# Kernel tuning notes

Hardware: AMD Instinct MI355X
Metric: run time of the kernel (lower is better)

## Reference

```python
import jax, jax.numpy as jnp
import numpy as np

N, F, H, R, E = 50000, 128, 128, 8, 800000
BN_EPS = 1e-5


def setup_inputs() -> dict:
    key = jax.random.key(0)
    ks = jax.random.split(key, 10)
    g = lambda k, shp: jax.random.normal(k, shp, dtype=jnp.float32) * (1.0 / np.sqrt(shp[-2] if len(shp) > 1 else shp[-1]))
    return {
        "x": jax.random.normal(ks[0], (N, F), dtype=jnp.float32),
        "edge_index": jax.random.randint(ks[1], (2, E), 0, N, dtype=jnp.int32),
        "edge_type": jax.random.randint(ks[2], (E,), 0, R, dtype=jnp.int32),
        "W1": g(ks[3], (F, H)),
        "b1": jnp.zeros((H,), jnp.float32),
        "weight": g(ks[4], (R, H, H)),
        "root": g(ks[5], (H, H)),
        "bias_c": jnp.zeros((H,), jnp.float32),
        "gamma": jnp.ones((H,), jnp.float32),
        "beta": jnp.zeros((H,), jnp.float32),
        "W2": g(ks[6], (H, H)),
        "b2": jnp.zeros((H,), jnp.float32),
        "Wo": g(ks[7], (H, 1)),
        "bo": jnp.zeros((1,), jnp.float32),
    }


def reference(x, edge_index, edge_type, W1, b1, weight, root, bias_c, gamma, beta, W2, b2, Wo, bo):
    n = x.shape[0]
    r = weight.shape[0]
    src, dst = edge_index[0], edge_index[1]
    # segment id combining relation and destination node: equivalent to the
    # per-relation edge-mask + scatter-add loop in RGCNConv, but in one pass.
    seg = edge_type.astype(jnp.int32) * n + dst

    def conv(h):
        msg = h[src]                                            # [E, H] gather
        agg = jax.ops.segment_sum(msg, seg, num_segments=r * n)  # [R*N, H]
        agg = agg.reshape(r, n, -1)                             # [R, N, H]
        out = jnp.einsum('rnc,rco->no', agg, weight)            # per-relation matmul, summed
        return out + h @ root + bias_c

    def bn(h):
        mu = h.mean(axis=0)
        var = h.var(axis=0)  # biased var, matches torch BN training normalization
        return gamma * (h - mu) * jax.lax.rsqrt(var + BN_EPS) + beta

    h = x @ W1 + b1
    h = jax.nn.relu(bn(conv(h)))
    h = jax.nn.relu(bn(conv(h)))
    h = h @ W2 + b2
    h = h @ Wo + bo
    return jax.nn.sigmoid(h)
```

## Files before the change

kernel.cpp:

```cpp
#include <hip/hip_runtime.h>
#include <stdint.h>

typedef __bf16 bf16;
typedef __bf16 bf16x8 __attribute__((ext_vector_type(8)));
typedef float f32x4 __attribute__((ext_vector_type(4)));

__device__ __forceinline__ float bfbits2f(uint32_t lo16) {
    uint32_t b = lo16 << 16;
    float f;
    __builtin_memcpy(&f, &b, 4);
    return f;
}

__device__ __forceinline__ uint32_t pack2bf(float a, float b) {
    uint32_t lo = __builtin_bit_cast(unsigned short, (bf16)a);
    uint32_t hi = __builtin_bit_cast(unsigned short, (bf16)b);
    return lo | (hi << 16);
}

__device__ __forceinline__ void gload_lds16(const void* g, void* l) {
    __builtin_amdgcn_global_load_lds((const __attribute__((address_space(1))) void*)g,
                                     (__attribute__((address_space(3))) void*)l, 16, 0, 0);
}

__global__ void k_prep(const float* __restrict__ W1, const float* __restrict__ weight,
                       const float* __restrict__ root, const float* __restrict__ W2,
                       const float* __restrict__ b2, const float* __restrict__ Wo,
                       const float* __restrict__ bo, bf16* __restrict__ W1T,
                       bf16* __restrict__ WcatT2, float* __restrict__ qc, int R, int ldt) {
    int total = 16384 * (R + 2);
    for (int i = blockIdx.x * blockDim.x + threadIdx.x; i < total + 129; i += gridDim.x * blockDim.x) {
        if (i < 16384) {
            int f = i >> 7, h = i & 127;
            W1T[h * 128 + f] = (bf16)W1[f * 128 + h];
        } else if (i < total) {
            int j = i - 16384;
            int r = j >> 14, rem = j & 16383, c = rem >> 7, o = rem & 127;
            float v = (r < R) ? weight[(size_t)(r * 128 + c) * 128 + o] : root[c * 128 + o];
            WcatT2[(size_t)o * ldt + r * 128 + c] = (bf16)v;
        } else {
            int t = i - total;
            if (t < 128) {
                float s = 0.f;
                for (int j = 0; j < 128; j++) s += W2[t * 128 + j] * Wo[j];
                qc[t] = s;
            } else {
                float c = bo[0];
                for (int j = 0; j < 128; j++) c += b2[j] * Wo[j];
                qc[128] = c;
            }
        }
    }
}

__global__ void k_hist(const int* __restrict__ dst, int* __restrict__ cnt, int E) {
    for (int e = blockIdx.x * blockDim.x + threadIdx.x; e < E; e += gridDim.x * blockDim.x)
        atomicAdd(&cnt[dst[e]], 1);
}

__global__ __launch_bounds__(256) void k_scan_blk(const int* __restrict__ cnt, int* __restrict__ bsum, int N) {
    int i = blockIdx.x * 256 + threadIdx.x;
    int v = (i < N) ? cnt[i] : 0;
#pragma unroll
    for (int d = 1; d < 64; d <<= 1) v += __shfl_xor(v, d);
    __shared__ int ws[4];
    if ((threadIdx.x & 63) == 0) ws[threadIdx.x >> 6] = v;
    __syncthreads();
    if (threadIdx.x == 0) bsum[blockIdx.x] = ws[0] + ws[1] + ws[2] + ws[3];
}

__global__ __launch_bounds__(256) void k_scan_top(int* __restrict__ bsum, int nb) {
    __shared__ int s[256];
    int t = threadIdx.x;
    int v = (t < nb) ? bsum[t] : 0;
    s[t] = v;
    __syncthreads();
#pragma unroll
    for (int d = 1; d < 256; d <<= 1) {
        int u = (t >= d) ? s[t - d] : 0;
        __syncthreads();
        s[t] += u;
        __syncthreads();
    }
    if (t < nb) bsum[t] = s[t] - v;
}

__global__ __launch_bounds__(256) void k_scan_apply(const int* __restrict__ cnt, const int* __restrict__ bsum,
                                                    int* __restrict__ row_off, int* __restrict__ cursor, int N) {
    int b = blockIdx.x, t = threadIdx.x;
    int i = b * 256 + t;
    int v = (i < N) ? cnt[i] : 0;
    int lane = t & 63, wid = t >> 6;
    int incl = v;
#pragma unroll
    for (int d = 1; d < 64; d <<= 1) {
        int u = __shfl_up(incl, d);
        if (lane >= d) incl += u;
    }
    __shared__ int ws[4];
    if (lane == 63) ws[wid] = incl;
    __syncthreads();
    int woff = 0;
    for (int wj = 0; wj < 4; wj++)
        if (wj < wid) woff += ws[wj];
    int excl = bsum[b] + woff + incl - v;
    if (i < N) {
        row_off[i] = excl;
        cursor[i] = excl;
        if (i == N - 1) row_off[N] = excl + v;
    }
}

__global__ void k_fill(const int* __restrict__ src, const int* __restrict__ dst,
                       const int* __restrict__ etype, int* __restrict__ cursor,
                       int* __restrict__ csr, int E, int pbase) {
    int p = blockIdx.x & 7;
    int bg = blockIdx.x >> 3;
    int nchunk = gridDim.x >> 3;
    int chunk = (E + nchunk - 1) / nchunk;
    int beg = bg * chunk, end = min(beg + chunk, E);
    int lo = p * pbase, hi = lo + pbase;
    for (int e = beg + (int)threadIdx.x; e < end; e += blockDim.x) {
        int d = dst[e];
        if (d >= lo && d < hi) {
            int pos = atomicAdd(&cursor[d], 1);
            csr[pos] = (etype[e] << 16) | src[e];
        }
    }
}

__global__ __launch_bounds__(256) void k_gemm0(const float* __restrict__ A, const bf16* __restrict__ BT,
                                               const float* __restrict__ bias, bf16* __restrict__ C, int M) {
    __shared__ bf16 sA[128 * 128];
    __shared__ bf16 sB[128 * 128];
    int tid = threadIdx.x;
    int m0 = blockIdx.x * 128;
#pragma unroll
    for (int i = 0; i < 8; i++) {
        int chunk = i * 256 + tid;
        int row = chunk >> 4, c16 = chunk & 15;
        int sw = ((c16 ^ (row & 7)) << 3);
        int gr = m0 + row;
        int4 va = {0, 0, 0, 0};
        if (gr < M) {
            const float* ap = A + (size_t)gr * 128 + (c16 << 3);
            float4 f0 = *reinterpret_cast<const float4*>(ap);
            float4 f1 = *reinterpret_cast<const float4*>(ap + 4);
            bf16 tmp[8] = {(bf16)f0.x, (bf16)f0.y, (bf16)f0.z, (bf16)f0.w,
                           (bf16)f1.x, (bf16)f1.y, (bf16)f1.z, (bf16)f1.w};
            __builtin_memcpy(&va, tmp, 16);
        }
        *reinterpret_cast<int4*>(&sA[row * 128 + sw]) = va;
        int4 vb = *reinterpret_cast<const int4*>(&BT[(size_t)row * 128 + (c16 << 3)]);
        *reinterpret_cast<int4*>(&sB[row * 128 + sw]) = vb;
    }
    __syncthreads();

    int lane = tid & 63, w = tid >> 6;
    int wm = (w >> 1) * 64, wn = (w & 1) * 64;
    int lr = lane & 15, lk = lane >> 4;
    f32x4 zero = {0.f, 0.f, 0.f, 0.f};
    f32x4 acc[4][4];
#pragma unroll
    for (int mi = 0; mi < 4; mi++)
#pragma unroll
        for (int ni = 0; ni < 4; ni++) acc[mi][ni] = zero;

#pragma unroll
    for (int kk = 0; kk < 4; kk++) {
        int c = (kk << 2) + lk;
        bf16x8 af[4], bfr[4];
#pragma unroll
        for (int mi = 0; mi < 4; mi++) {
            int r = wm + mi * 16 + lr;
            af[mi] = *reinterpret_cast<const bf16x8*>(&sA[r * 128 + ((c ^ (r & 7)) << 3)]);
        }
#pragma unroll
        for (int ni = 0; ni < 4; ni++) {
            int r = wn + ni * 16 + lr;
            bfr[ni] = *reinterpret_cast<const bf16x8*>(&sB[r * 128 + ((c ^ (r & 7)) << 3)]);
        }
#pragma unroll
        for (int mi = 0; mi < 4; mi++)
#pragma unroll
            for (int ni = 0; ni < 4; ni++)
                acc[mi][ni] = __builtin_amdgcn_mfma_f32_16x16x32_bf16(af[mi], bfr[ni], acc[mi][ni], 0, 0, 0);
    }

#pragma unroll
    for (int ni = 0; ni < 4; ni++) {
        int col = wn + ni * 16 + lr;
        float bia = bias[col];
#pragma unroll
        for (int mi = 0; mi < 4; mi++) {
#pragma unroll
            for (int j = 0; j < 4; j++) {
                int row = m0 + wm + mi * 16 + lk * 4 + j;
                if (row < M) C[(size_t)row * 128 + col] = (bf16)(acc[mi][ni][j] + bia);
            }
        }
    }
}

__global__ __launch_bounds__(128) void k_agg2(const bf16* __restrict__ h, const int* __restrict__ row_off,
                                              const int* __restrict__ csr, bf16* __restrict__ G, int N) {
    __shared__ float acc[2][8 * 128];
    int wi = threadIdx.x >> 6;
    int n = blockIdx.x * 2 + wi;
    if (n >= N) return;
    int lane = threadIdx.x & 63;
    int c0 = lane * 2;
    float* a = acc[wi];
#pragma unroll
    for (int i = 0; i < 16; i++) a[i * 64 + lane] = 0.f;
    int beg = row_off[n], end = row_off[n + 1];
    int i = beg;
    for (; i + 4 <= end; i += 4) {
        int p0 = csr[i], p1 = csr[i + 1], p2 = csr[i + 2], p3 = csr[i + 3];
        uint32_t v0 = *reinterpret_cast<const uint32_t*>(&h[(size_t)(p0 & 0xffff) * 128 + c0]);
        uint32_t v1 = *reinterpret_cast<const uint32_t*>(&h[(size_t)(p1 & 0xffff) * 128 + c0]);
        uint32_t v2 = *reinterpret_cast<const uint32_t*>(&h[(size_t)(p2 & 0xffff) * 128 + c0]);
        uint32_t v3 = *reinterpret_cast<const uint32_t*>(&h[(size_t)(p3 & 0xffff) * 128 + c0]);
        float* a0 = &a[(p0 >> 16) * 128 + c0];
        a0[0] += bfbits2f(v0 & 0xffffu); a0[1] += bfbits2f(v0 >> 16);
        float* a1 = &a[(p1 >> 16) * 128 + c0];
        a1[0] += bfbits2f(v1 & 0xffffu); a1[1] += bfbits2f(v1 >> 16);
        float* a2 = &a[(p2 >> 16) * 128 + c0];
        a2[0] += bfbits2f(v2 & 0xffffu); a2[1] += bfbits2f(v2 >> 16);
        float* a3 = &a[(p3 >> 16) * 128 + c0];
        a3[0] += bfbits2f(v3 & 0xffffu); a3[1] += bfbits2f(v3 >> 16);
    }
    for (; i < end; i++) {
        int p = csr[i];
        uint32_t v = *reinterpret_cast<const uint32_t*>(&h[(size_t)(p & 0xffff) * 128 + c0]);
        float* ap = &a[(p >> 16) * 128 + c0];
        ap[0] += bfbits2f(v & 0xffffu);
        ap[1] += bfbits2f(v >> 16);
    }
    size_t gbase = (size_t)n * 1024 + c0;
#pragma unroll
    for (int r = 0; r < 8; r++) {
        __builtin_nontemporal_store(pack2bf(a[r * 128 + c0], a[r * 128 + c0 + 1]),
                                    reinterpret_cast<uint32_t*>(&G[gbase + r * 128]));
    }
}

__global__ __launch_bounds__(256) void k_gemm2(const bf16* __restrict__ G, const bf16* __restrict__ hsrc,
                                               const bf16* __restrict__ BT, const float* __restrict__ bias,
                                               float* __restrict__ C, float* __restrict__ stats,
                                               int M, int K) {
    __shared__ bf16 sA[128 * 128];
    __shared__ bf16 sB[128 * 128];
    __shared__ float csum[128], csum2[128];
    int tid = threadIdx.x;
    if (tid < 128) { csum[tid] = 0.f; csum2[tid] = 0.f; }
    int m0 = blockIdx.x * 128;
    int lane = tid & 63, w = tid >> 6;
    int wm = (w >> 1) * 64, wn = (w & 1) * 64;
    int lr = lane & 15, lk = lane >> 4;
    int l4 = lane >> 4, c16 = lane & 15;
    f32x4 zero = {0.f, 0.f, 0.f, 0.f};
    f32x4 acc[4][4];
#pragma unroll
    for (int mi = 0; mi < 4; mi++)
#pragma unroll
        for (int ni = 0; ni < 4; ni++) acc[mi][ni] = zero;

    int KT = K >> 7;
    size_t ldg = (size_t)(K - 128);
    for (int kt = 0; kt < KT; kt++) {
        bool lastt = (kt == KT - 1);
        const bf16* Abase = lastt ? hsrc : G;
        size_t ldA = lastt ? 128 : ldg;
        int ka = lastt ? 0 : (kt << 7);
        int k0 = kt << 7;
#pragma unroll
        for (int i = 0; i < 8; i++) {
            int row = i * 16 + (w << 2) + l4;
            int cs = (c16 ^ (row & 7)) << 3;
            int gr = m0 + row;
            gr = gr < M ? gr : M - 1;
            gload_lds16(Abase + (size_t)gr * ldA + ka + cs, &sA[(i * 256 + (w << 6)) * 8]);
            gload_lds16(&BT[(size_t)row * K + k0 + cs], &sB[(i * 256 + (w << 6)) * 8]);
        }
        asm volatile("s_waitcnt vmcnt(0)" ::: "memory");
        __syncthreads();

#pragma unroll
        for (int kk = 0; kk < 4; kk++) {
            int c = (kk << 2) + lk;
            bf16x8 af[4], bfr[4];
#pragma unroll
            for (int mi = 0; mi < 4; mi++) {
                int r = wm + mi * 16 + lr;
                af[mi] = *reinterpret_cast<const bf16x8*>(&sA[r * 128 + ((c ^ (r & 7)) << 3)]);
            }
#pragma unroll
            for (int ni = 0; ni < 4; ni++) {
                int r = wn + ni * 16 + lr;
                bfr[ni] = *reinterpret_cast<const bf16x8*>(&sB[r * 128 + ((c ^ (r & 7)) << 3)]);
            }
#pragma unroll
            for (int mi = 0; mi < 4; mi++)
#pragma unroll
                for (int ni = 0; ni < 4; ni++)
                    acc[mi][ni] = __builtin_amdgcn_mfma_f32_16x16x32_bf16(af[mi], bfr[ni], acc[mi][ni], 0, 0, 0);
        }
        __syncthreads();
    }

    float ls[4], ls2[4];
#pragma unroll
    for (int ni = 0; ni < 4; ni++) { ls[ni] = 0.f; ls2[ni] = 0.f; }
#pragma unroll
    for (int ni = 0; ni < 4; ni++) {
        int col = wn + ni * 16 + lr;
        float bia = bias[col];
#pragma unroll
        for (int mi = 0; mi < 4; mi++) {
#pragma unroll
            for (int j = 0; j < 4; j++) {
                int row = m0 + wm + mi * 16 + lk * 4 + j;
                if (row < M) {
                    float val = acc[mi][ni][j] + bia;
                    C[(size_t)row * 128 + col] = val;
                    ls[ni] += val;
                    ls2[ni] += val * val;
                }
            }
        }
    }
#pragma unroll
    for (int ni = 0; ni < 4; ni++) {
        float s = ls[ni], s2 = ls2[ni];
        s += __shfl_xor(s, 16); s += __shfl_xor(s, 32);
        s2 += __shfl_xor(s2, 16); s2 += __shfl_xor(s2, 32);
        if (lk == 0) {
            int col = wn + ni * 16 + lr;
            atomicAdd(&csum[col], s);
            atomicAdd(&csum2[col], s2);
        }
    }
    __syncthreads();
    if (tid < 128) {
        atomicAdd(&stats[tid], csum[tid]);
        atomicAdd(&stats[128 + tid], csum2[tid]);
    }
}

__global__ void k_bnfin(float* __restrict__ stats, const float* __restrict__ gamma,
                        const float* __restrict__ beta, float* __restrict__ bnp, float invN) {
    int t = threadIdx.x;
    float mu = stats[t] * invN;
    float var = stats[128 + t] * invN - mu * mu;
    float sc = gamma[t] * rsqrtf(var + 1e-5f);
    bnp[t] = sc;
    bnp[128 + t] = beta[t] - mu * sc;
    stats[t] = 0.f;
    stats[128 + t] = 0.f;
}

__global__ void k_bnrelu(const float* __restrict__ conv, const float* __restrict__ bnp,
                         bf16* __restrict__ h, int N) {
    int total = N * 32;
    for (int i = blockIdx.x * blockDim.x + threadIdx.x; i < total; i += gridDim.x * blockDim.x) {
        int c4 = (i & 31) << 2;
        float4 v = *reinterpret_cast<const float4*>(&conv[(size_t)i * 4]);
        const float* vv = &v.x;
        uint64_t pk = 0;
#pragma unroll
        for (int j = 0; j < 4; j++) {
            int c = c4 + j;
            float val = fmaxf(vv[j] * bnp[c] + bnp[128 + c], 0.f);
            unsigned short us = __builtin_bit_cast(unsigned short, (bf16)val);
            pk |= (uint64_t)us << (16 * j);
        }
        *reinterpret_cast<uint64_t*>(&h[(size_t)i * 4]) = pk;
    }
}

__global__ __launch_bounds__(256) void k_bnout(const float* __restrict__ conv, const float* __restrict__ bnp,
                                               const float* __restrict__ qc, float* __restrict__ out, int N) {
    int wi = threadIdx.x >> 6;
    int n = blockIdx.x * 4 + wi;
    if (n >= N) return;
    int lane = threadIdx.x & 63;
    int c0 = lane * 2;
    float2 v = *reinterpret_cast<const float2*>(&conv[(size_t)n * 128 + c0]);
    float v0 = fmaxf(v.x * bnp[c0] + bnp[128 + c0], 0.f);
    float v1 = fmaxf(v.y * bnp[c0 + 1] + bnp[128 + c0 + 1], 0.f);
    float s = v0 * qc[c0] + v1 * qc[c0 + 1];
#pragma unroll
    for (int d = 1; d < 64; d <<= 1) s += __shfl_xor(s, d);
    if (lane == 0) out[n] = 1.f / (1.f + expf(-(s + qc[128])));
}

extern "C" void kernel_launch(void* const* d_in, const int* in_sizes, int n_in,
                              void* d_out, int out_size, void* d_ws, size_t ws_size,
                              hipStream_t stream) {
    const float* x      = (const float*)d_in[0];
    const int*   ei     = (const int*)d_in[1];
    const int*   etype  = (const int*)d_in[2];
    const float* W1     = (const float*)d_in[3];
    const float* b1     = (const float*)d_in[4];
    const float* weight = (const float*)d_in[5];
    const float* root   = (const float*)d_in[6];
    const float* bias_c = (const float*)d_in[7];
    const float* gamma  = (const float*)d_in[8];
    const float* beta   = (const float*)d_in[9];
    const float* W2     = (const float*)d_in[10];
    const float* b2     = (const float*)d_in[11];
    const float* Wo     = (const float*)d_in[12];
    const float* bo     = (const float*)d_in[13];
    float* out = (float*)d_out;

    int H = in_sizes[4];
    int F = in_sizes[3] / H;
    int N = in_sizes[0] / F;
    int E = in_sizes[2];
    int R = in_sizes[5] / (H * H);
    int ldt = (R + 1) * H;

    const int* srcv = ei;
    const int* dstv = ei + E;

    char* p = (char*)d_ws;
    auto alloc = [&](size_t bytes) -> char* {
        char* r = p;
        p += (bytes + 255) & ~(size_t)255;
        return r;
    };
    bf16*  G       = (bf16*)alloc((size_t)N * (R * H) * 2);
    bf16*  h       = (bf16*)alloc((size_t)N * H * 2);
    float* conv    = (float*)alloc((size_t)N * H * 4);
    bf16*  WcatT2  = (bf16*)alloc((size_t)ldt * H * 2);
    bf16*  W1T     = (bf16*)alloc((size_t)F * H * 2);
    float* qc      = (float*)alloc(129 * 4);
    int*   cnt     = (int*)alloc((size_t)N * 4);
    int*   row_off = (int*)alloc((size_t)(N + 1) * 4);
    int*   cursor  = (int*)alloc((size_t)N * 4);
    int*   csr     = (int*)alloc((size_t)E * 4);
    float* stats   = (float*)alloc(256 * 4);
    float* bnp     = (float*)alloc(256 * 4);
    int*   bsum    = (int*)alloc(256 * 4);
    if ((size_t)(p - (char*)d_ws) > ws_size) return;

    int nb = (N + 255) / 256;
    int pbase = (N + 7) / 8;

    hipMemsetAsync(cnt, 0, (size_t)N * 4, stream);
    hipMemsetAsync(stats, 0, 256 * 4, stream);
    k_prep<<<256, 256, 0, stream>>>(W1, weight, root, W2, b2, Wo, bo, W1T, WcatT2, qc, R, ldt);
    k_hist<<<1024, 256, 0, stream>>>(dstv, cnt, E);
    k_scan_blk<<<nb, 256, 0, stream>>>(cnt, bsum, N);
    k_scan_top<<<1, 256, 0, stream>>>(bsum, nb);
    k_scan_apply<<<nb, 256, 0, stream>>>(cnt, bsum, row_off, cursor, N);
    k_fill<<<1024, 256, 0, stream>>>(srcv, dstv, etype, cursor, csr, E, pbase);

    int mb = (N + 127) / 128;
    k_gemm0<<<mb, 256, 0, stream>>>(x, W1T, b1, h, N);

    for (int l = 0; l < 2; l++) {
        k_agg2<<<(N + 1) / 2, 128, 0, stream>>>(h, row_off, csr, G, N);
        k_gemm2<<<mb, 256, 0, stream>>>(G, h, WcatT2, bias_c, conv, stats, N, ldt);
        k_bnfin<<<1, 128, 0, stream>>>(stats, gamma, beta, bnp, 1.f / (float)N);
        if (l == 0)
            k_bnrelu<<<2048, 256, 0, stream>>>(conv, bnp, h, N);
        else
            k_bnout<<<(N + 3) / 4, 256, 0, stream>>>(conv, bnp, qc, out, N);
    }
}
```

Baseline: 303.0 us.

## Transform node features per relation before aggregation instead of after

Reorders the RGCN conv to first compute h·W_r for all relations plus root in one dense GEMM (N×1152 bf16), then gathers and sums the pre-transformed rows per edge into registers, adding root and bias. This removes the per-node LDS scatter into 8 relation slots and the wide K=1152 GEMM over the aggregated G buffer. BN statistics move into a separate pass over conv. In exchange it adds an extra read of conv for stats, and each gathered row now comes from a larger HW table, so random reads hit a wider working set.

Measured after the change: 327.6 us. 8.1% more time.

```diff
diff --git a/kernel.cpp b/kernel.cpp
--- a/kernel.cpp
+++ b/kernel.cpp
@@ -12,12 +12,6 @@
     return f;
 }
 
-__device__ __forceinline__ uint32_t pack2bf(float a, float b) {
-    uint32_t lo = __builtin_bit_cast(unsigned short, (bf16)a);
-    uint32_t hi = __builtin_bit_cast(unsigned short, (bf16)b);
-    return lo | (hi << 16);
-}
-
 __device__ __forceinline__ void gload_lds16(const void* g, void* l) {
     __builtin_amdgcn_global_load_lds((const __attribute__((address_space(1))) void*)g,
                                      (__attribute__((address_space(3))) void*)l, 16, 0, 0);
@@ -27,7 +21,7 @@
                        const float* __restrict__ root, const float* __restrict__ W2,
                        const float* __restrict__ b2, const float* __restrict__ Wo,
                        const float* __restrict__ bo, bf16* __restrict__ W1T,
-                       bf16* __restrict__ WcatT2, float* __restrict__ qc, int R, int ldt) {
+                       bf16* __restrict__ WhwT, float* __restrict__ qc, int R) {
     int total = 16384 * (R + 2);
     for (int i = blockIdx.x * blockDim.x + threadIdx.x; i < total + 129; i += gridDim.x * blockDim.x) {
         if (i < 16384) {
@@ -35,9 +29,9 @@
             W1T[h * 128 + f] = (bf16)W1[f * 128 + h];
         } else if (i < total) {
             int j = i - 16384;
-            int r = j >> 14, rem = j & 16383, c = rem >> 7, o = rem & 127;
-            float v = (r < R) ? weight[(size_t)(r * 128 + c) * 128 + o] : root[c * 128 + o];
-            WcatT2[(size_t)o * ldt + r * 128 + c] = (bf16)v;
+            int r = j >> 14, rem = j & 16383, c = rem >> 7, k = rem & 127;
+            float v = (r < R) ? weight[((size_t)(r * 128 + k)) * 128 + c] : root[(size_t)k * 128 + c];
+            WhwT[(size_t)(r * 128 + c) * 128 + k] = (bf16)v;
         } else {
             int t = i - total;
             if (t < 128) {
@@ -202,149 +196,143 @@
     }
 }
 
-__global__ __launch_bounds__(128) void k_agg2(const bf16* __restrict__ h, const int* __restrict__ row_off,
-                                              const int* __restrict__ csr, bf16* __restrict__ G, int N) {
-    __shared__ float acc[2][8 * 128];
+__global__ __launch_bounds__(256) void k_hwgemm(const bf16* __restrict__ h, const bf16* __restrict__ WhwT,
+                                                bf16* __restrict__ HW, int M, int NS) {
+    __shared__ bf16 sA[128 * 128];
+    __shared__ bf16 sB[128 * 128];
+    int tid = threadIdx.x;
+    int m0 = blockIdx.x * 128;
+    int lane = tid & 63, w = tid >> 6;
+    int l4 = lane >> 4, c16 = lane & 15;
+    int wm = (w >> 1) * 64, wn = (w & 1) * 64;
+    int lr = lane & 15, lk = lane >> 4;
+    int ldhw = NS * 128;
+
+#pragma unroll
+    for (int i = 0; i < 8; i++) {
+        int row = i * 16 + (w << 2) + l4;
+        int cs = (c16 ^ (row & 7)) << 3;
+        int gr = m0 + row;
+        gr = gr < M ? gr : M - 1;
+        gload_lds16(h + (size_t)gr * 128 + cs, &sA[(i * 256 + (w << 6)) * 8]);
+    }
+    asm volatile("s_waitcnt vmcnt(0)" ::: "memory");
+    __syncthreads();
+
+    bf16x8 af[4][4];
+#pragma unroll
+    for (int kk = 0; kk < 4; kk++) {
+        int c = (kk << 2) + lk;
+#pragma unroll
+        for (int mi = 0; mi < 4; mi++) {
+            int r = wm + mi * 16 + lr;
+            af[kk][mi] = *reinterpret_cast<const bf16x8*>(&sA[r * 128 + ((c ^ (r & 7)) << 3)]);
+        }
+    }
+    __syncthreads();
+
+    for (int ns = 0; ns < NS; ns++) {
+#pragma unroll
+        for (int i = 0; i < 8; i++) {
+            int row = i * 16 + (w << 2) + l4;
+            int cs = (c16 ^ (row & 7)) << 3;
+            gload_lds16(WhwT + (size_t)(ns * 128 + row) * 128 + cs, &sB[(i * 256 + (w << 6)) * 8]);
+        }
+        asm volatile("s_waitcnt vmcnt(0)" ::: "memory");
+        __syncthreads();
+
+        f32x4 zero = {0.f, 0.f, 0.f, 0.f};
+        f32x4 acc[4][4];
+#pragma unroll
+        for (int mi = 0; mi < 4; mi++)
+#pragma unroll
+            for (int ni = 0; ni < 4; ni++) acc[mi][ni] = zero;
+
+#pragma unroll
+        for (int kk = 0; kk < 4; kk++) {
+            int c = (kk << 2) + lk;
+            bf16x8 bfr[4];
+#pragma unroll
+            for (int ni = 0; ni < 4; ni++) {
+                int r = wn + ni * 16 + lr;
+                bfr[ni] = *reinterpret_cast<const bf16x8*>(&sB[r * 128 + ((c ^ (r & 7)) << 3)]);
+            }
+#pragma unroll
+            for (int mi = 0; mi < 4; mi++)
+#pragma unroll
+                for (int ni = 0; ni < 4; ni++)
+                    acc[mi][ni] = __builtin_amdgcn_mfma_f32_16x16x32_bf16(af[kk][mi], bfr[ni], acc[mi][ni], 0, 0, 0);
+        }
+
+#pragma unroll
+        for (int ni = 0; ni < 4; ni++) {
+            int col = ns * 128 + wn + ni * 16 + lr;
+#pragma unroll
+            for (int mi = 0; mi < 4; mi++) {
+#pragma unroll
+                for (int j = 0; j < 4; j++) {
+                    int row = m0 + wm + mi * 16 + lk * 4 + j;
+                    if (row < M) HW[(size_t)row * ldhw + col] = (bf16)acc[mi][ni][j];
+                }
+            }
+        }
+        __syncthreads();
+    }
+}
+
+__global__ __launch_bounds__(128) void k_agg3(const bf16* __restrict__ HW, const int* __restrict__ row_off,
+                                              const int* __restrict__ csr, const float* __restrict__ bias,
+                                              float* __restrict__ conv, int N, int ldhw, int R) {
     int wi = threadIdx.x >> 6;
     int n = blockIdx.x * 2 + wi;
     if (n >= N) return;
     int lane = threadIdx.x & 63;
     int c0 = lane * 2;
-    float* a = acc[wi];
-#pragma unroll
-    for (int i = 0; i < 16; i++) a[i * 64 + lane] = 0.f;
+    float a0 = 0.f, a1 = 0.f;
     int beg = row_off[n], end = row_off[n + 1];
     int i = beg;
     for (; i + 4 <= end; i += 4) {
         int p0 = csr[i], p1 = csr[i + 1], p2 = csr[i + 2], p3 = csr[i + 3];
-        uint32_t v0 = *reinterpret_cast<const uint32_t*>(&h[(size_t)(p0 & 0xffff) * 128 + c0]);
-        uint32_t v1 = *reinterpret_cast<const uint32_t*>(&h[(size_t)(p1 & 0xffff) * 128 + c0]);
-        uint32_t v2 = *reinterpret_cast<const uint32_t*>(&h[(size_t)(p2 & 0xffff) * 128 + c0]);
-        uint32_t v3 = *reinterpret_cast<const uint32_t*>(&h[(size_t)(p3 & 0xffff) * 128 + c0]);
-        float* a0 = &a[(p0 >> 16) * 128 + c0];
-        a0[0] += bfbits2f(v0 & 0xffffu); a0[1] += bfbits2f(v0 >> 16);
-        float* a1 = &a[(p1 >> 16) * 128 + c0];
-        a1[0] += bfbits2f(v1 & 0xffffu); a1[1] += bfbits2f(v1 >> 16);
-        float* a2 = &a[(p2 >> 16) * 128 + c0];
-        a2[0] += bfbits2f(v2 & 0xffffu); a2[1] += bfbits2f(v2 >> 16);
-        float* a3 = &a[(p3 >> 16) * 128 + c0];
-        a3[0] += bfbits2f(v3 & 0xffffu); a3[1] += bfbits2f(v3 >> 16);
+        uint32_t v0 = *reinterpret_cast<const uint32_t*>(&HW[(size_t)(p0 & 0xffff) * ldhw + ((p0 >> 16) << 7) + c0]);
+        uint32_t v1 = *reinterpret_cast<const uint32_t*>(&HW[(size_t)(p1 & 0xffff) * ldhw + ((p1 >> 16) << 7) + c0]);
+        uint32_t v2 = *reinterpret_cast<const uint32_t*>(&HW[(size_t)(p2 & 0xffff) * ldhw + ((p2 >> 16) << 7) + c0]);
+        uint32_t v3 = *reinterpret_cast<const uint32_t*>(&HW[(size_t)(p3 & 0xffff) * ldhw + ((p3 >> 16) << 7) + c0]);
+        a0 += bfbits2f(v0 & 0xffffu); a1 += bfbits2f(v0 >> 16);
+        a0 += bfbits2f(v1 & 0xffffu); a1 += bfbits2f(v1 >> 16);
+        a0 += bfbits2f(v2 & 0xffffu); a1 += bfbits2f(v2 >> 16);
+        a0 += bfbits2f(v3 & 0xffffu); a1 += bfbits2f(v3 >> 16);
     }
     for (; i < end; i++) {
         int p = csr[i];
-        uint32_t v = *reinterpret_cast<const uint32_t*>(&h[(size_t)(p & 0xffff) * 128 + c0]);
-        float* ap = &a[(p >> 16) * 128 + c0];
-        ap[0] += bfbits2f(v & 0xffffu);
-        ap[1] += bfbits2f(v >> 16);
-    }
-    size_t gbase = (size_t)n * 1024 + c0;
-#pragma unroll
-    for (int r = 0; r < 8; r++) {
-        __builtin_nontemporal_store(pack2bf(a[r * 128 + c0], a[r * 128 + c0 + 1]),
-                                    reinterpret_cast<uint32_t*>(&G[gbase + r * 128]));
-    }
-}
-
-__global__ __launch_bounds__(256) void k_gemm2(const bf16* __restrict__ G, const bf16* __restrict__ hsrc,
-                                               const bf16* __restrict__ BT, const float* __restrict__ bias,
-                                               float* __restrict__ C, float* __restrict__ stats,
-                                               int M, int K) {
-    __shared__ bf16 sA[128 * 128];
-    __shared__ bf16 sB[128 * 128];
-    __shared__ float csum[128], csum2[128];
+        uint32_t v = *reinterpret_cast<const uint32_t*>(&HW[(size_t)(p & 0xffff) * ldhw + ((p >> 16) << 7) + c0]);
+        a0 += bfbits2f(v & 0xffffu); a1 += bfbits2f(v >> 16);
+    }
+    uint32_t vr = *reinterpret_cast<const uint32_t*>(&HW[(size_t)n * ldhw + (R << 7) + c0]);
+    a0 += bfbits2f(vr & 0xffffu) + bias[c0];
+    a1 += bfbits2f(vr >> 16) + bias[c0 + 1];
+    float2 st = {a0, a1};
+    *reinterpret_cast<float2*>(&conv[(size_t)n * 128 + c0]) = st;
+}
+
+__global__ __launch_bounds__(256) void k_stats(const float* __restrict__ conv, float* __restrict__ stats, int N) {
+    __shared__ float cs[128], cs2[128];
     int tid = threadIdx.x;
-    if (tid < 128) { csum[tid] = 0.f; csum2[tid] = 0.f; }
-    int m0 = blockIdx.x * 128;
-    int lane = tid & 63, w = tid >> 6;
-    int wm = (w >> 1) * 64, wn = (w & 1) * 64;
-    int lr = lane & 15, lk = lane >> 4;
-    int l4 = lane >> 4, c16 = lane & 15;
-    f32x4 zero = {0.f, 0.f, 0.f, 0.f};
-    f32x4 acc[4][4];
-#pragma unroll
-    for (int mi = 0; mi < 4; mi++)
-#pragma unroll
-        for (int ni = 0; ni < 4; ni++) acc[mi][ni] = zero;
-
-    int KT = K >> 7;
-    size_t ldg = (size_t)(K - 128);
-    for (int kt = 0; kt < KT; kt++) {
-        bool lastt = (kt == KT - 1);
-        const bf16* Abase = lastt ? hsrc : G;
-        size_t ldA = lastt ? 128 : ldg;
-        int ka = lastt ? 0 : (kt << 7);
-        int k0 = kt << 7;
-#pragma unroll
-        for (int i = 0; i < 8; i++) {
-            int row = i * 16 + (w << 2) + l4;
-            int cs = (c16 ^ (row & 7)) << 3;
-            int gr = m0 + row;
-            gr = gr < M ? gr : M - 1;
-            gload_lds16(Abase + (size_t)gr * ldA + ka + cs, &sA[(i * 256 + (w << 6)) * 8]);
-            gload_lds16(&BT[(size_t)row * K + k0 + cs], &sB[(i * 256 + (w << 6)) * 8]);
-        }
-        asm volatile("s_waitcnt vmcnt(0)" ::: "memory");
-        __syncthreads();
-
-#pragma unroll
-        for (int kk = 0; kk < 4; kk++) {
-            int c = (kk << 2) + lk;
-            bf16x8 af[4], bfr[4];
-#pragma unroll
-            for (int mi = 0; mi < 4; mi++) {
-                int r = wm + mi * 16 + lr;
-                af[mi] = *reinterpret_cast<const bf16x8*>(&sA[r * 128 + ((c ^ (r & 7)) << 3)]);
-            }
-#pragma unroll
-            for (int ni = 0; ni < 4; ni++) {
-                int r = wn + ni * 16 + lr;
-                bfr[ni] = *reinterpret_cast<const bf16x8*>(&sB[r * 128 + ((c ^ (r & 7)) << 3)]);
-            }
-#pragma unroll
-            for (int mi = 0; mi < 4; mi++)
-#pragma unroll
-                for (int ni = 0; ni < 4; ni++)
-                    acc[mi][ni] = __builtin_amdgcn_mfma_f32_16x16x32_bf16(af[mi], bfr[ni], acc[mi][ni], 0, 0, 0);
-        }
-        __syncthreads();
-    }
-
-    float ls[4], ls2[4];
-#pragma unroll
-    for (int ni = 0; ni < 4; ni++) { ls[ni] = 0.f; ls2[ni] = 0.f; }
-#pragma unroll
-    for (int ni = 0; ni < 4; ni++) {
-        int col = wn + ni * 16 + lr;
-        float bia = bias[col];
-#pragma unroll
-        for (int mi = 0; mi < 4; mi++) {
-#pragma unroll
-            for (int j = 0; j < 4; j++) {
-                int row = m0 + wm + mi * 16 + lk * 4 + j;
-                if (row < M) {
-                    float val = acc[mi][ni][j] + bia;
-                    C[(size_t)row * 128 + col] = val;
-                    ls[ni] += val;
-                    ls2[ni] += val * val;
-                }
-            }
-        }
-    }
-#pragma unroll
-    for (int ni = 0; ni < 4; ni++) {
-        float s = ls[ni], s2 = ls2[ni];
-        s += __shfl_xor(s, 16); s += __shfl_xor(s, 32);
-        s2 += __shfl_xor(s2, 16); s2 += __shfl_xor(s2, 32);
-        if (lk == 0) {
-            int col = wn + ni * 16 + lr;
-            atomicAdd(&csum[col], s);
-            atomicAdd(&csum2[col], s2);
-        }
-    }
+    if (tid < 128) { cs[tid] = 0.f; cs2[tid] = 0.f; }
+    __syncthreads();
+    int c = (tid & 63) * 2;
+    int rg = tid >> 6;
+    float s0 = 0.f, s20 = 0.f, s1 = 0.f, s21 = 0.f;
+    for (int row = blockIdx.x * 4 + rg; row < N; row += gridDim.x * 4) {
+        float2 v = *reinterpret_cast<const float2*>(&conv[(size_t)row * 128 + c]);
+        s0 += v.x; s20 += v.x * v.x;
+        s1 += v.y; s21 += v.y * v.y;
+    }
+    atomicAdd(&cs[c], s0); atomicAdd(&cs[c + 1], s1);
+    atomicAdd(&cs2[c], s20); atomicAdd(&cs2[c + 1], s21);
     __syncthreads();
     if (tid < 128) {
-        atomicAdd(&stats[tid], csum[tid]);
-        atomicAdd(&stats[128 + tid], csum2[tid]);
+        atomicAdd(&stats[tid], cs[tid]);
+        atomicAdd(&stats[128 + tid], cs2[tid]);
     }
 }
 
@@ -419,7 +407,8 @@
     int N = in_sizes[0] / F;
     int E = in_sizes[2];
     int R = in_sizes[5] / (H * H);
-    int ldt = (R + 1) * H;
+    int NS = R + 1;
+    int ldhw = NS * H;
 
     const int* srcv = ei;
     const int* dstv = ei + E;
@@ -430,10 +419,10 @@
         p += (bytes + 255) & ~(size_t)255;
         return r;
     };
-    bf16*  G       = (bf16*)alloc((size_t)N * (R * H) * 2);
+    bf16*  HW      = (bf16*)alloc((size_t)N * ldhw * 2);
     bf16*  h       = (bf16*)alloc((size_t)N * H * 2);
     float* conv    = (float*)alloc((size_t)N * H * 4);
-    bf16*  WcatT2  = (bf16*)alloc((size_t)ldt * H * 2);
+    bf16*  WhwT    = (bf16*)alloc((size_t)ldhw * H * 2);
     bf16*  W1T     = (bf16*)alloc((size_t)F * H * 2);
     float* qc      = (float*)alloc(129 * 4);
     int*   cnt     = (int*)alloc((size_t)N * 4);
@@ -450,7 +439,7 @@
 
     hipMemsetAsync(cnt, 0, (size_t)N * 4, stream);
     hipMemsetAsync(stats, 0, 256 * 4, stream);
-    k_prep<<<256, 256, 0, stream>>>(W1, weight, root, W2, b2, Wo, bo, W1T, WcatT2, qc, R, ldt);
+    k_prep<<<256, 256, 0, stream>>>(W1, weight, root, W2, b2, Wo, bo, W1T, WhwT, qc, R);
     k_hist<<<1024, 256, 0, stream>>>(dstv, cnt, E);
     k_scan_blk<<<nb, 256, 0, stream>>>(cnt, bsum, N);
     k_scan_top<<<1, 256, 0, stream>>>(bsum, nb);
@@ -461,8 +450,9 @@
     k_gemm0<<<mb, 256, 0, stream>>>(x, W1T, b1, h, N);
 
     for (int l = 0; l < 2; l++) {
-        k_agg2<<<(N + 1) / 2, 128, 0, stream>>>(h, row_off, csr, G, N);
-        k_gemm2<<<mb, 256, 0, stream>>>(G, h, WcatT2, bias_c, conv, stats, N, ldt);
+        k_hwgemm<<<mb, 256, 0, stream>>>(h, WhwT, HW, N, NS);
+        k_agg3<<<(N + 1) / 2, 128, 0, stream>>>(HW, row_off, csr, bias_c, conv, N, ldhw, R);
+        k_stats<<<512, 256, 0, stream>>>(conv, stats, N);
         k_bnfin<<<1, 128, 0, stream>>>(stats, gamma, beta, bnp, 1.f / (float)N);
         if (l == 0)
             k_bnrelu<<<2048, 256, 0, stream>>>(conv, bnp, h, N);
```

## Double-buffer GEMM K-tiles with async global-to-LDS loads in k_gemm2

Applied to the files above, without the earlier changes.

Restructures the k_gemm2 main loop from a single 128-wide K tile per iteration with a full vmcnt(0) wait into two 64-wide K-tile LDS buffers, prefetching two stages ahead. It waits with vmcnt(8) so the next tile's loads stay in flight while the current tile is consumed by MFMA. The goal is to overlap global memory latency with compute. In exchange there are more barriers per K step, and the loop now depends on the 8-loads-per-stage count matching the vmcnt value.

After: 306.4 us. Within noise of the previous version (+1.1%).

```diff
diff --git a/kernel.cpp b/kernel.cpp
--- a/kernel.cpp
+++ b/kernel.cpp
@@ -249,8 +249,8 @@
                                                const bf16* __restrict__ BT, const float* __restrict__ bias,
                                                float* __restrict__ C, float* __restrict__ stats,
                                                int M, int K) {
-    __shared__ bf16 sA[128 * 128];
-    __shared__ bf16 sB[128 * 128];
+    __shared__ bf16 sA[2][128 * 64];
+    __shared__ bf16 sB[2][128 * 64];
     __shared__ float csum[128], csum2[128];
     int tid = threadIdx.x;
     if (tid < 128) { csum[tid] = 0.f; csum2[tid] = 0.f; }
@@ -258,7 +258,35 @@
     int lane = tid & 63, w = tid >> 6;
     int wm = (w >> 1) * 64, wn = (w & 1) * 64;
     int lr = lane & 15, lk = lane >> 4;
-    int l4 = lane >> 4, c16 = lane & 15;
+    int KT = K >> 6;
+    int KG = (K - 128) >> 6;
+    size_t ldg = (size_t)(K - 128);
+
+    int rowi[4], csi[4], grA[4];
+#pragma unroll
+    for (int i = 0; i < 4; i++) {
+        int chunkid = i * 256 + tid;
+        rowi[i] = chunkid >> 3;
+        csi[i] = ((chunkid & 7) ^ (rowi[i] & 7)) << 3;
+        int g = m0 + rowi[i];
+        grA[i] = g < M ? g : M - 1;
+    }
+
+    auto stage = [&](int kt, int b) {
+        bool lastt = (kt >= KG);
+        const bf16* Abase = lastt ? hsrc : G;
+        size_t ldA = lastt ? 128 : ldg;
+        int ka = lastt ? ((kt - KG) << 6) : (kt << 6);
+        int k0 = kt << 6;
+        bf16* dA = &sA[b][(w << 6) * 8];
+        bf16* dB = &sB[b][(w << 6) * 8];
+#pragma unroll
+        for (int i = 0; i < 4; i++) {
+            gload_lds16(Abase + (size_t)grA[i] * ldA + ka + csi[i], dA + i * 2048);
+            gload_lds16(&BT[(size_t)rowi[i] * K + k0 + csi[i]], dB + i * 2048);
+        }
+    };
+
     f32x4 zero = {0.f, 0.f, 0.f, 0.f};
     f32x4 acc[4][4];
 #pragma unroll
@@ -266,39 +294,30 @@
 #pragma unroll
         for (int ni = 0; ni < 4; ni++) acc[mi][ni] = zero;
 
-    int KT = K >> 7;
-    size_t ldg = (size_t)(K - 128);
+    stage(0, 0);
+    stage(1, 1);
     for (int kt = 0; kt < KT; kt++) {
-        bool lastt = (kt == KT - 1);
-        const bf16* Abase = lastt ? hsrc : G;
-        size_t ldA = lastt ? 128 : ldg;
-        int ka = lastt ? 0 : (kt << 7);
-        int k0 = kt << 7;
-#pragma unroll
-        for (int i = 0; i < 8; i++) {
-            int row = i * 16 + (w << 2) + l4;
-            int cs = (c16 ^ (row & 7)) << 3;
-            int gr = m0 + row;
-            gr = gr < M ? gr : M - 1;
-            gload_lds16(Abase + (size_t)gr * ldA + ka + cs, &sA[(i * 256 + (w << 6)) * 8]);
-            gload_lds16(&BT[(size_t)row * K + k0 + cs], &sB[(i * 256 + (w << 6)) * 8]);
-        }
-        asm volatile("s_waitcnt vmcnt(0)" ::: "memory");
-        __syncthreads();
-
-#pragma unroll
-        for (int kk = 0; kk < 4; kk++) {
+        if (kt + 1 < KT)
+            asm volatile("s_waitcnt vmcnt(8)" ::: "memory");
+        else
+            asm volatile("s_waitcnt vmcnt(0)" ::: "memory");
+        __builtin_amdgcn_s_barrier();
+        int b = kt & 1;
+        const bf16* A = sA[b];
+        const bf16* B = sB[b];
+#pragma unroll
+        for (int kk = 0; kk < 2; kk++) {
             int c = (kk << 2) + lk;
             bf16x8 af[4], bfr[4];
 #pragma unroll
             for (int mi = 0; mi < 4; mi++) {
                 int r = wm + mi * 16 + lr;
-                af[mi] = *reinterpret_cast<const bf16x8*>(&sA[r * 128 + ((c ^ (r & 7)) << 3)]);
+                af[mi] = *reinterpret_cast<const bf16x8*>(&A[r * 64 + ((c ^ (r & 7)) << 3)]);
             }
 #pragma unroll
             for (int ni = 0; ni < 4; ni++) {
                 int r = wn + ni * 16 + lr;
-                bfr[ni] = *reinterpret_cast<const bf16x8*>(&sB[r * 128 + ((c ^ (r & 7)) << 3)]);
+                bfr[ni] = *reinterpret_cast<const bf16x8*>(&B[r * 64 + ((c ^ (r & 7)) << 3)]);
             }
 #pragma unroll
             for (int mi = 0; mi < 4; mi++)
@@ -306,7 +325,8 @@
                 for (int ni = 0; ni < 4; ni++)
                     acc[mi][ni] = __builtin_amdgcn_mfma_f32_16x16x32_bf16(af[mi], bfr[ni], acc[mi][ni], 0, 0, 0);
         }
-        __syncthreads();
+        __builtin_amdgcn_s_barrier();
+        if (kt + 2 < KT) stage(kt + 2, b);
     }
 
     float ls[4], ls2[4];
```

## Sort CSR edges by (dst, relation) to accumulate aggregation in registers

Applied to the files above, without the earlier changes.

The CSR build now histograms and scans over (destination, relation) segments, so each node's edges are grouped by relation. The aggregation kernel then keeps a running register sum per relation run and writes it to LDS, replacing read-modify-write LDS accumulation per edge. The cost is a scan that is R times larger, including a multi-pass top-level scan, more atomic cursor slots, and a larger histogram memset.

Result: no change. 304.0 us (+0.3%).

```diff
diff --git a/kernel.cpp b/kernel.cpp
--- a/kernel.cpp
+++ b/kernel.cpp
@@ -53,14 +53,15 @@
     }
 }
 
-__global__ void k_hist(const int* __restrict__ dst, int* __restrict__ cnt, int E) {
+__global__ void k_hist(const int* __restrict__ dst, const int* __restrict__ etype,
+                       int* __restrict__ cnt, int E, int R) {
     for (int e = blockIdx.x * blockDim.x + threadIdx.x; e < E; e += gridDim.x * blockDim.x)
-        atomicAdd(&cnt[dst[e]], 1);
-}
-
-__global__ __launch_bounds__(256) void k_scan_blk(const int* __restrict__ cnt, int* __restrict__ bsum, int N) {
+        atomicAdd(&cnt[dst[e] * R + etype[e]], 1);
+}
+
+__global__ __launch_bounds__(256) void k_scan_blk(const int* __restrict__ cnt, int* __restrict__ bsum, int M) {
     int i = blockIdx.x * 256 + threadIdx.x;
-    int v = (i < N) ? cnt[i] : 0;
+    int v = (i < M) ? cnt[i] : 0;
 #pragma unroll
     for (int d = 1; d < 64; d <<= 1) v += __shfl_xor(v, d);
     __shared__ int ws[4];
@@ -71,25 +72,36 @@
 
 __global__ __launch_bounds__(256) void k_scan_top(int* __restrict__ bsum, int nb) {
     __shared__ int s[256];
+    __shared__ int carry;
     int t = threadIdx.x;
-    int v = (t < nb) ? bsum[t] : 0;
-    s[t] = v;
+    if (t == 0) carry = 0;
     __syncthreads();
-#pragma unroll
-    for (int d = 1; d < 256; d <<= 1) {
-        int u = (t >= d) ? s[t - d] : 0;
+    for (int base = 0; base < nb; base += 256) {
+        int i = base + t;
+        int v = (i < nb) ? bsum[i] : 0;
+        s[t] = v;
         __syncthreads();
-        s[t] += u;
+#pragma unroll
+        for (int d = 1; d < 256; d <<= 1) {
+            int u = (t >= d) ? s[t - d] : 0;
+            __syncthreads();
+            s[t] += u;
+            __syncthreads();
+        }
+        int excl = carry + s[t] - v;
+        int tot = s[255];
         __syncthreads();
-    }
-    if (t < nb) bsum[t] = s[t] - v;
+        if (i < nb) bsum[i] = excl;
+        if (t == 0) carry += tot;
+        __syncthreads();
+    }
 }
 
 __global__ __launch_bounds__(256) void k_scan_apply(const int* __restrict__ cnt, const int* __restrict__ bsum,
-                                                    int* __restrict__ row_off, int* __restrict__ cursor, int N) {
+                                                    int* __restrict__ row_off, int* __restrict__ cursor, int M) {
     int b = blockIdx.x, t = threadIdx.x;
     int i = b * 256 + t;
-    int v = (i < N) ? cnt[i] : 0;
+    int v = (i < M) ? cnt[i] : 0;
     int lane = t & 63, wid = t >> 6;
     int incl = v;
 #pragma unroll
@@ -104,16 +116,16 @@
     for (int wj = 0; wj < 4; wj++)
         if (wj < wid) woff += ws[wj];
     int excl = bsum[b] + woff + incl - v;
-    if (i < N) {
+    if (i < M) {
         row_off[i] = excl;
         cursor[i] = excl;
-        if (i == N - 1) row_off[N] = excl + v;
+        if (i == M - 1) row_off[M] = excl + v;
     }
 }
 
 __global__ void k_fill(const int* __restrict__ src, const int* __restrict__ dst,
                        const int* __restrict__ etype, int* __restrict__ cursor,
-                       int* __restrict__ csr, int E, int pbase) {
+                       int* __restrict__ csr, int E, int R, int pbase) {
     int p = blockIdx.x & 7;
     int bg = blockIdx.x >> 3;
     int nchunk = gridDim.x >> 3;
@@ -121,10 +133,11 @@
     int beg = bg * chunk, end = min(beg + chunk, E);
     int lo = p * pbase, hi = lo + pbase;
     for (int e = beg + (int)threadIdx.x; e < end; e += blockDim.x) {
-        int d = dst[e];
-        if (d >= lo && d < hi) {
-            int pos = atomicAdd(&cursor[d], 1);
-            csr[pos] = (etype[e] << 16) | src[e];
+        int et = etype[e];
+        int seg = dst[e] * R + et;
+        if (seg >= lo && seg < hi) {
+            int pos = atomicAdd(&cursor[seg], 1);
+            csr[pos] = (et << 16) | src[e];
         }
     }
 }
@@ -203,7 +216,7 @@
 }
 
 __global__ __launch_bounds__(128) void k_agg2(const bf16* __restrict__ h, const int* __restrict__ row_off,
-                                              const int* __restrict__ csr, bf16* __restrict__ G, int N) {
+                                              const int* __restrict__ csr, bf16* __restrict__ G, int N, int R) {
     __shared__ float acc[2][8 * 128];
     int wi = threadIdx.x >> 6;
     int n = blockIdx.x * 2 + wi;
@@ -213,7 +226,9 @@
     float* a = acc[wi];
 #pragma unroll
     for (int i = 0; i < 16; i++) a[i * 64 + lane] = 0.f;
-    int beg = row_off[n], end = row_off[n + 1];
+    int beg = row_off[n * R], end = row_off[n * R + R];
+    int cur = -1;
+    float a0 = 0.f, a1 = 0.f;
     int i = beg;
     for (; i + 4 <= end; i += 4) {
         int p0 = csr[i], p1 = csr[i + 1], p2 = csr[i + 2], p3 = csr[i + 3];
@@ -221,21 +236,48 @@
         uint32_t v1 = *reinterpret_cast<const uint32_t*>(&h[(size_t)(p1 & 0xffff) * 128 + c0]);
         uint32_t v2 = *reinterpret_cast<const uint32_t*>(&h[(size_t)(p2 & 0xffff) * 128 + c0]);
         uint32_t v3 = *reinterpret_cast<const uint32_t*>(&h[(size_t)(p3 & 0xffff) * 128 + c0]);
-        float* a0 = &a[(p0 >> 16) * 128 + c0];
-        a0[0] += bfbits2f(v0 & 0xffffu); a0[1] += bfbits2f(v0 >> 16);
-        float* a1 = &a[(p1 >> 16) * 128 + c0];
-        a1[0] += bfbits2f(v1 & 0xffffu); a1[1] += bfbits2f(v1 >> 16);
-        float* a2 = &a[(p2 >> 16) * 128 + c0];
-        a2[0] += bfbits2f(v2 & 0xffffu); a2[1] += bfbits2f(v2 >> 16);
-        float* a3 = &a[(p3 >> 16) * 128 + c0];
-        a3[0] += bfbits2f(v3 & 0xffffu); a3[1] += bfbits2f(v3 >> 16);
+        {
+            int r = p0 >> 16; bool s = (r == cur);
+            a0 = (s ? a0 : 0.f) + bfbits2f(v0 & 0xffffu);
+            a1 = (s ? a1 : 0.f) + bfbits2f(v0 >> 16);
+            cur = r;
+            float2 st = {a0, a1};
+            *reinterpret_cast<float2*>(&a[r * 128 + c0]) = st;
+        }
+        {
+            int r = p1 >> 16; bool s = (r == cur);
+            a0 = (s ? a0 : 0.f) + bfbits2f(v1 & 0xffffu);
+            a1 = (s ? a1 : 0.f) + bfbits2f(v1 >> 16);
+            cur = r;
+            float2 st = {a0, a1};
+            *reinterpret_cast<float2*>(&a[r * 128 + c0]) = st;
+        }
+        {
+            int r = p2 >> 16; bool s = (r == cur);
+            a0 = (s ? a0 : 0.f) + bfbits2f(v2 & 0xffffu);
+            a1 = (s ? a1 : 0.f) + bfbits2f(v2 >> 16);
+            cur = r;
+            float2 st = {a0, a1};
+            *reinterpret_cast<float2*>(&a[r * 128 + c0]) = st;
+        }
+        {
+            int r = p3 >> 16; bool s = (r == cur);
+            a0 = (s ? a0 : 0.f) + bfbits2f(v3 & 0xffffu);
+            a1 = (s ? a1 : 0.f) + bfbits2f(v3 >> 16);
+            cur = r;
+            float2 st = {a0, a1};
+            *reinterpret_cast<float2*>(&a[r * 128 + c0]) = st;
+        }
     }
     for (; i < end; i++) {
         int p = csr[i];
         uint32_t v = *reinterpret_cast<const uint32_t*>(&h[(size_t)(p & 0xffff) * 128 + c0]);
-        float* ap = &a[(p >> 16) * 128 + c0];
-        ap[0] += bfbits2f(v & 0xffffu);
-        ap[1] += bfbits2f(v >> 16);
+        int r = p >> 16; bool s = (r == cur);
+        a0 = (s ? a0 : 0.f) + bfbits2f(v & 0xffffu);
+        a1 = (s ? a1 : 0.f) + bfbits2f(v >> 16);
+        cur = r;
+        float2 st = {a0, a1};
+        *reinterpret_cast<float2*>(&a[r * 128 + c0]) = st;
     }
     size_t gbase = (size_t)n * 1024 + c0;
 #pragma unroll
@@ -420,6 +462,7 @@
     int E = in_sizes[2];
     int R = in_sizes[5] / (H * H);
     int ldt = (R + 1) * H;
+    int M = N * R;
 
     const int* srcv = ei;
     const int* dstv = ei + E;
@@ -436,32 +479,32 @@
     bf16*  WcatT2  = (bf16*)alloc((size_t)ldt * H * 2);
     bf16*  W1T     = (bf16*)alloc((size_t)F * H * 2);
     float* qc      = (float*)alloc(129 * 4);
-    int*   cnt     = (int*)alloc((size_t)N * 4);
-    int*   row_off = (int*)alloc((size_t)(N + 1) * 4);
-    int*   cursor  = (int*)alloc((size_t)N * 4);
+    int*   cnt     = (int*)alloc((size_t)M * 4);
+    int*   row_off = (int*)alloc((size_t)(M + 1) * 4);
+    int*   cursor  = (int*)alloc((size_t)M * 4);
     int*   csr     = (int*)alloc((size_t)E * 4);
     float* stats   = (float*)alloc(256 * 4);
     float* bnp     = (float*)alloc(256 * 4);
-    int*   bsum    = (int*)alloc(256 * 4);
+    int*   bsum    = (int*)alloc(2048 * 4);
     if ((size_t)(p - (char*)d_ws) > ws_size) return;
 
-    int nb = (N + 255) / 256;
-    int pbase = (N + 7) / 8;
-
-    hipMemsetAsync(cnt, 0, (size_t)N * 4, stream);
+    int nb = (M + 255) / 256;
+    int pbase = (M + 7) / 8;
+
+    hipMemsetAsync(cnt, 0, (size_t)M * 4, stream);
     hipMemsetAsync(stats, 0, 256 * 4, stream);
     k_prep<<<256, 256, 0, stream>>>(W1, weight, root, W2, b2, Wo, bo, W1T, WcatT2, qc, R, ldt);
-    k_hist<<<1024, 256, 0, stream>>>(dstv, cnt, E);
-    k_scan_blk<<<nb, 256, 0, stream>>>(cnt, bsum, N);
+    k_hist<<<1024, 256, 0, stream>>>(dstv, etype, cnt, E, R);
+    k_scan_blk<<<nb, 256, 0, stream>>>(cnt, bsum, M);
     k_scan_top<<<1, 256, 0, stream>>>(bsum, nb);
-    k_scan_apply<<<nb, 256, 0, stream>>>(cnt, bsum, row_off, cursor, N);
-    k_fill<<<1024, 256, 0, stream>>>(srcv, dstv, etype, cursor, csr, E, pbase);
+    k_scan_apply<<<nb, 256, 0, stream>>>(cnt, bsum, row_off, cursor, M);
+    k_fill<<<1024, 256, 0, stream>>>(srcv, dstv, etype, cursor, csr, E, R, pbase);
 
     int mb = (N + 127) / 128;
     k_gemm0<<<mb, 256, 0, stream>>>(x, W1T, b1, h, N);
 
     for (int l = 0; l < 2; l++) {
-        k_agg2<<<(N + 1) / 2, 128, 0, stream>>>(h, row_off, csr, G, N);
+        k_agg2<<<(N + 1) / 2, 128, 0, stream>>>(h, row_off, csr, G, N, R);
         k_gemm2<<<mb, 256, 0, stream>>>(G, h, WcatT2, bias_c, conv, stats, N, ldt);
         k_bnfin<<<1, 128, 0, stream>>>(stats, gamma, beta, bnp, 1.f / (float)N);
         if (l == 0)
```
